# Optimization experiments

Hardware: AMD Instinct MI355X
Metric: run time of the kernel (lower is better)

Reference implementation:

```python
import jax, jax.numpy as jnp
import numpy as np
from functools import partial

BATCH, SEQ = 2, 2048
D_MODEL, D_INNER, D_XB = 2048, 4096, 1024
HEADDIM, D_STATE = 64, 64
NHEADS = D_INNER // HEADDIM      # 64
NKV = D_XB // HEADDIM            # 16
REP = NHEADS // NKV              # 4
INTER = 8192
EPS = 1e-5
D_IN_PROJ = D_INNER + D_XB + D_XB + D_INNER + NHEADS  # z, x, B, C, dt


def setup_inputs() -> dict:
    key = jax.random.key(0)
    ks = jax.random.split(key, 8)
    g = lambda k, shape, s: (jax.random.normal(k, shape, jnp.float32) * s)
    return {
        "hidden_states": g(ks[0], (BATCH, SEQ, D_MODEL), 1.0),
        "ln_w": jnp.ones((D_MODEL,), jnp.float32),
        "ln_b": jnp.zeros((D_MODEL,), jnp.float32),
        "in_proj_w": g(ks[1], (D_IN_PROJ, D_MODEL), 0.02),
        "dt_bias": jax.random.uniform(ks[2], (NHEADS,), jnp.float32, -4.0, 0.0),
        "A_log": jnp.log(jnp.arange(1, NHEADS + 1, dtype=jnp.float32)),
        "Dp": jnp.ones((NHEADS,), jnp.float32),
        "norm_w": jnp.ones((D_INNER,), jnp.float32),
        "out_proj_w": g(ks[3], (D_MODEL, D_INNER), 0.02),
        "fc1_w": g(ks[4], (INTER, D_MODEL), 0.02),
        "fc1_b": jnp.zeros((INTER,), jnp.float32),
        "fc2_w": g(ks[5], (D_MODEL, INTER), 0.02),
        "fc2_b": jnp.zeros((D_MODEL,), jnp.float32),
    }


def _layernorm(x, w, b):
    mu = x.mean(-1, keepdims=True)
    var = ((x - mu) ** 2).mean(-1, keepdims=True)
    return (x - mu) * jax.lax.rsqrt(var + EPS) * w + b


def _ssd_scan(xh, dt, A, Bh, Ch):
    # xh: (b,l,h,p)  dt: (b,l,h)  A: (h,)  Bh,Ch: (b,l,h,n)
    dA = jnp.exp(dt * A)  # (b,l,h) discrete decay
    to_l = lambda t: jnp.moveaxis(t, 1, 0)  # time-major for scan

    def step(state, inp):
        dA_t, dt_t, x_t, B_t, C_t = inp
        state = state * dA_t[:, :, None, None] + jnp.einsum(
            "bh,bhp,bhn->bhpn", dt_t, x_t, B_t)
        y = jnp.einsum("bhpn,bhn->bhp", state, C_t)
        return state, y

    state0 = jnp.zeros((xh.shape[0], NHEADS, HEADDIM, D_STATE), xh.dtype)
    _, ys = jax.lax.scan(step, state0, (to_l(dA), to_l(dt), to_l(xh), to_l(Bh), to_l(Ch)))
    return jnp.moveaxis(ys, 0, 1)  # (b,l,h,p)


def reference(hidden_states, ln_w, ln_b, in_proj_w, dt_bias, A_log, Dp,
              norm_w, out_proj_w, fc1_w, fc1_b, fc2_w, fc2_b):
    residual = hidden_states
    h = _layernorm(hidden_states, ln_w, ln_b)

    # ---- Mamba2 branch ----
    zxbcdt = h @ in_proj_w.T  # (b,l,D_IN_PROJ)
    z, x, Bm, Cm, dt = jnp.split(
        zxbcdt, np.cumsum([D_INNER, D_XB, D_XB, D_INNER]).tolist(), axis=-1)
    b, l = h.shape[0], h.shape[1]
    dt = jax.nn.softplus(dt + dt_bias)               # (b,l,nheads)
    A = -jnp.exp(A_log)                              # (nheads,)
    # GQA-style repeat of x (values) and B (keys) from NKV to NHEADS groups
    xh = jnp.repeat(x.reshape(b, l, NKV, HEADDIM), REP, axis=2)   # (b,l,h,p)
    Bh = jnp.repeat(Bm.reshape(b, l, NKV, D_STATE), REP, axis=2)  # (b,l,h,n)
    Ch = Cm.reshape(b, l, NHEADS, D_STATE)                        # (b,l,h,n)

    y = _ssd_scan(xh, dt, A, Bh, Ch) + Dp[None, None, :, None] * xh
    yf = y.reshape(b, l, D_INNER)
    # gated RMSNorm (norm_before_gate=False): gate first, then rmsnorm
    yf = yf * jax.nn.silu(z)
    yf = yf * jax.lax.rsqrt((yf * yf).mean(-1, keepdims=True) + EPS) * norm_w
    mamba_out = yf @ out_proj_w.T

    # ---- Phi MLP branch (parallel, shares the layernormed input) ----
    mlp = jax.nn.gelu(h @ fc1_w.T + fc1_b, approximate=True) @ fc2_w.T + fc2_b

    # resid_dropout is identity in eval mode
    return mamba_out + mlp + residual
```

## Files before the change

### kernel.cpp

```cpp
#include <hip/hip_runtime.h>
#include <hip/hip_bf16.h>

#define BATCH 2
#define SEQ   2048
#define DMODEL 2048
#define DINNER 4096
#define DXB   1024
#define NHEADS 64
#define NKV   16
#define HEADDIM 64
#define DSTATE 64
#define INTER 8192
#define DINPROJ 10304
#define ROWS  (BATCH*SEQ)
#define NC    32
#define EPSV  1e-5f

typedef short short8 __attribute__((ext_vector_type(8)));
typedef float f32x4 __attribute__((ext_vector_type(4)));

typedef const __attribute__((address_space(1))) unsigned int cg_u32;
typedef __attribute__((address_space(3))) unsigned int ls_u32;

static __device__ __forceinline__ void gll16(const void* g, void* l) {
    __builtin_amdgcn_global_load_lds((cg_u32*)g, (ls_u32*)l, 16, 0, 0);
}

static __device__ __forceinline__ unsigned short f2bf(float f) {
    unsigned int u = __float_as_uint(f);
    unsigned int r = (u + 0x7fffu + ((u >> 16) & 1u)) >> 16;
    return (unsigned short)r;
}
static __device__ __forceinline__ float bf2f(unsigned short h) {
    return __uint_as_float(((unsigned int)h) << 16);
}

__global__ __launch_bounds__(256) void convk(const float* __restrict__ in,
                                             unsigned short* __restrict__ out, int n4) {
    int stride = gridDim.x * blockDim.x;
    for (int i = blockIdx.x * blockDim.x + threadIdx.x; i < n4; i += stride) {
        float4 v = ((const float4*)in)[i];
        ushort4 o;
        o.x = f2bf(v.x); o.y = f2bf(v.y); o.z = f2bf(v.z); o.w = f2bf(v.w);
        ((ushort4*)out)[i] = o;
    }
}

__global__ __launch_bounds__(256) void ln_kernel(const float* __restrict__ x,
                                                 const float* __restrict__ w,
                                                 const float* __restrict__ b,
                                                 unsigned short* __restrict__ hout) {
    int row = blockIdx.x;
    int t = threadIdx.x;
    const float* xr = x + (size_t)row * DMODEL;
    float v[8];
    float4 v0 = *(const float4*)&xr[t * 8];
    float4 v1 = *(const float4*)&xr[t * 8 + 4];
    v[0]=v0.x; v[1]=v0.y; v[2]=v0.z; v[3]=v0.w; v[4]=v1.x; v[5]=v1.y; v[6]=v1.z; v[7]=v1.w;
    float s = 0.f, s2 = 0.f;
    #pragma unroll
    for (int i = 0; i < 8; ++i) { s += v[i]; s2 += v[i]*v[i]; }
    #pragma unroll
    for (int off = 1; off < 64; off <<= 1) { s += __shfl_xor(s, off); s2 += __shfl_xor(s2, off); }
    __shared__ float sa[4], sb[4];
    int lane = t & 63, wv = t >> 6;
    if (lane == 0) { sa[wv] = s; sb[wv] = s2; }
    __syncthreads();
    s = sa[0]+sa[1]+sa[2]+sa[3];
    s2 = sb[0]+sb[1]+sb[2]+sb[3];
    float mu = s / DMODEL;
    float var = s2 / DMODEL - mu * mu;
    float sc = rsqrtf(var + EPSV);
    unsigned short* ho = hout + (size_t)row * DMODEL + t * 8;
    #pragma unroll
    for (int i = 0; i < 8; ++i) {
        int d = t * 8 + i;
        ho[i] = f2bf((v[i] - mu) * sc * w[d] + b[d]);
    }
}

#define SLOTSZ 49152
template <int EPI>
__global__ __launch_bounds__(512, 2) void gemm_p(
    const unsigned short* __restrict__ A, const unsigned short* __restrict__ B,
    int M, int N, int K, int nby,
    float* __restrict__ outF, unsigned short* __restrict__ outH,
    const float* __restrict__ bias, const float* __restrict__ add1,
    const float* __restrict__ add2) {
    __shared__ __align__(16) char smem[3 * SLOTSZ];
    int t = threadIdx.x, lane = t & 63, w = t >> 6;
    int nwg = gridDim.x, cpx = nwg >> 3;
    int logical = (blockIdx.x & 7) * cpx + (blockIdx.x >> 3);
    int by = logical % nby, bx = logical / nby;
    int brow = by * 128, bcol = bx * 256;
    int wr = w >> 2, wc = w & 3;
    int wrb = wr * 64, wcb = wc * 64;

    int lr8 = lane >> 3;
    int lch = ((lane & 7) ^ lr8) << 3;
    const unsigned short* pa[2];
    #pragma unroll
    for (int j = 0; j < 2; ++j)
        pa[j] = A + (size_t)(brow + w * 16 + j * 8 + lr8) * K + lch;
    const unsigned short* pb[4];
    #pragma unroll
    for (int j = 0; j < 4; ++j) {
        int r = bcol + w * 32 + j * 8 + lr8;
        if (r > N - 1) r = N - 1;
        pb[j] = B + (size_t)r * K + lch;
    }
    auto stageA = [&](int slot, int j) {
        gll16(pa[j], smem + slot * SLOTSZ + (w * 16 + j * 8) * 128);
        pa[j] += 64;
    };
    auto stageB = [&](int slot, int j) {
        gll16(pb[j], smem + slot * SLOTSZ + 16384 + (w * 32 + j * 8) * 128);
        pb[j] += 64;
    };

    int arow = lane & 15;
    int swz0 = (((lane >> 4) ^ (lane & 7)) << 4);

    f32x4 acc[4][4] = {};
    const int NT = K >> 6;
    #pragma unroll
    for (int j = 0; j < 2; ++j) stageA(0, j);
    #pragma unroll
    for (int j = 0; j < 4; ++j) stageB(0, j);
    #pragma unroll
    for (int j = 0; j < 2; ++j) stageA(1, j);
    #pragma unroll
    for (int j = 0; j < 4; ++j) stageB(1, j);

    int slot = 0, slot2 = 2;
    for (int kt = 0; kt < NT; ++kt) {
        if (kt + 1 < NT) { asm volatile("s_waitcnt vmcnt(6)" ::: "memory"); }
        else             { asm volatile("s_waitcnt vmcnt(0)" ::: "memory"); }
        __builtin_amdgcn_s_barrier();
        asm volatile("" ::: "memory");
        const char* Ab = smem + slot * SLOTSZ;
        const char* Bb = Ab + 16384;
        bool st = (kt + 2 < NT);
        short8 af[4], bfv[4];
        #pragma unroll
        for (int f = 0; f < 4; ++f)
            af[f] = *(const short8*)(Ab + (wrb + f * 16 + arow) * 128 + swz0);
        #pragma unroll
        for (int n = 0; n < 4; ++n)
            bfv[n] = *(const short8*)(Bb + (wcb + n * 16 + arow) * 128 + swz0);
        if (st) { stageA(slot2, 0); stageA(slot2, 1); stageB(slot2, 0); }
        __builtin_amdgcn_s_setprio(1);
        #pragma unroll
        for (int f = 0; f < 4; ++f)
            #pragma unroll
            for (int n = 0; n < 4; ++n)
                acc[f][n] = __builtin_amdgcn_mfma_f32_16x16x32_bf16(af[f], bfv[n], acc[f][n], 0, 0, 0);
        __builtin_amdgcn_s_setprio(0);
        #pragma unroll
        for (int f = 0; f < 4; ++f)
            af[f] = *(const short8*)(Ab + (wrb + f * 16 + arow) * 128 + (swz0 ^ 64));
        #pragma unroll
        for (int n = 0; n < 4; ++n)
            bfv[n] = *(const short8*)(Bb + (wcb + n * 16 + arow) * 128 + (swz0 ^ 64));
        if (st) { stageB(slot2, 1); stageB(slot2, 2); stageB(slot2, 3); }
        __builtin_amdgcn_s_setprio(1);
        #pragma unroll
        for (int f = 0; f < 4; ++f)
            #pragma unroll
            for (int n = 0; n < 4; ++n)
                acc[f][n] = __builtin_amdgcn_mfma_f32_16x16x32_bf16(af[f], bfv[n], acc[f][n], 0, 0, 0);
        __builtin_amdgcn_s_setprio(0);
        slot  = (slot  == 2) ? 0 : slot + 1;
        slot2 = (slot2 == 2) ? 0 : slot2 + 1;
    }

    int rlane = (lane >> 4) << 2, clane = lane & 15;
    #pragma unroll
    for (int f = 0; f < 4; ++f) {
        #pragma unroll
        for (int n = 0; n < 4; ++n) {
            int col = bcol + wcb + n * 16 + clane;
            if (col < N) {
                #pragma unroll
                for (int j = 0; j < 4; ++j) {
                    int row = brow + wrb + f * 16 + rlane + j;
                    size_t idx = (size_t)row * N + col;
                    float v = acc[f][n][j];
                    if constexpr (EPI == 0) {
                        outF[idx] = v;
                    } else if constexpr (EPI == 1) {
                        v += bias[col];
                        float g = 0.5f * v * (1.f + tanhf(0.7978845608f * (v + 0.044715f * v * v * v)));
                        outH[idx] = f2bf(g);
                    } else if constexpr (EPI == 2) {
                        outF[idx] = v + bias[col] + add1[idx] + add2[idx];
                    } else {
                        outH[idx] = f2bf(v);
                    }
                }
            }
        }
    }
}

static __device__ __forceinline__ void mm64(const unsigned short* Al, const unsigned short* Bl,
                                            f32x4* acc, int w, int lane) {
    int lr = lane & 15, kg = (lane >> 4) << 3;
    #pragma unroll
    for (int ks = 0; ks < 2; ++ks) {
        short8 a = *(const short8*)&Al[(w * 16 + lr) * 64 + ks * 32 + kg];
        #pragma unroll
        for (int fn = 0; fn < 4; ++fn) {
            short8 bb = *(const short8*)&Bl[(fn * 16 + lr) * 64 + ks * 32 + kg];
            acc[fn] = __builtin_amdgcn_mfma_f32_16x16x32_bf16(a, bb, acc[fn], 0, 0, 0);
        }
    }
}

__global__ __launch_bounds__(256) void chunk_front(const unsigned short* __restrict__ zx,
                                                   const float* __restrict__ dt_bias,
                                                   const float* __restrict__ A_log,
                                                   float* __restrict__ pcum,
                                                   unsigned short* __restrict__ ybuf,
                                                   unsigned short* __restrict__ Sbuf) {
    __shared__ __align__(16) unsigned short Cs[64*64], Bsr[64*64], Btr[64*64],
                                            Xtr[64*64], Xw[64*64], Wsm[64*64];
    __shared__ float dts[64], clg[64];
    int t = threadIdx.x, lane = t & 63, w = t >> 6;
    int bid = blockIdx.x;
    int c = bid & 31, h = (bid >> 5) & 63, b = bid >> 11, g = h >> 2;
    int row0 = (b << 11) + (c << 6);

    if (t < 64) {
        float raw = bf2f(zx[(size_t)(row0 + t) * DINPROJ + 10240 + h]) + dt_bias[h];
        float dt = raw > 20.f ? raw : log1pf(expf(raw));
        dts[t] = dt;
        float v = dt * (-expf(A_log[h]));
        #pragma unroll
        for (int off = 1; off < 64; off <<= 1) {
            float o = __shfl_up(v, off);
            if (lane >= off) v += o;
        }
        clg[t] = v;
        pcum[(size_t)(row0 + t) * 64 + h] = expf(v);
    }
    ushort4 xr[4];
    #pragma unroll
    for (int i = 0; i < 4; ++i) {
        int q = i * 256 + t, s = q >> 4, d4 = (q & 15) << 2;
        const unsigned short* rp = zx + (size_t)(row0 + s) * DINPROJ;
        ushort4 cv = *(const ushort4*)&rp[6144 + h * 64 + d4];
        *(ushort4*)&Cs[s * 64 + d4] = cv;
        ushort4 bv = *(const ushort4*)&rp[5120 + g * 64 + d4];
        *(ushort4*)&Bsr[s * 64 + d4] = bv;
        Btr[(d4 + 0) * 64 + s] = bv.x; Btr[(d4 + 1) * 64 + s] = bv.y;
        Btr[(d4 + 2) * 64 + s] = bv.z; Btr[(d4 + 3) * 64 + s] = bv.w;
        ushort4 xv = *(const ushort4*)&rp[4096 + g * 64 + d4];
        Xtr[(d4 + 0) * 64 + s] = xv.x; Xtr[(d4 + 1) * 64 + s] = xv.y;
        Xtr[(d4 + 2) * 64 + s] = xv.z; Xtr[(d4 + 3) * 64 + s] = xv.w;
        xr[i] = xv;
    }
    __syncthreads();
    float cl63 = clg[63];
    #pragma unroll
    for (int i = 0; i < 4; ++i) {
        int q = i * 256 + t, s = q >> 4, d4 = (q & 15) << 2;
        float ws = dts[s] * expf(cl63 - clg[s]);
        Xw[(d4 + 0) * 64 + s] = f2bf(bf2f(xr[i].x) * ws);
        Xw[(d4 + 1) * 64 + s] = f2bf(bf2f(xr[i].y) * ws);
        Xw[(d4 + 2) * 64 + s] = f2bf(bf2f(xr[i].z) * ws);
        Xw[(d4 + 3) * 64 + s] = f2bf(bf2f(xr[i].w) * ws);
    }
    __syncthreads();
    f32x4 accG[4] = {};
    mm64(Cs, Bsr, accG, w, lane);
    int rl = (lane >> 4) << 2, cl = lane & 15;
    #pragma unroll
    for (int fn = 0; fn < 4; ++fn) {
        #pragma unroll
        for (int j = 0; j < 4; ++j) {
            int tr = w * 16 + rl + j, rc = fn * 16 + cl;
            float val = 0.f;
            if (rc <= tr) val = accG[fn][j] * expf(clg[tr] - clg[rc]) * dts[rc];
            Wsm[tr * 64 + rc] = f2bf(val);
        }
    }
    __syncthreads();
    f32x4 accY[4] = {};
    mm64(Wsm, Xtr, accY, w, lane);
    f32x4 accS[4] = {};
    mm64(Xw, Btr, accS, w, lane);
    size_t cb = (size_t)((((b << 6) + h) << 5) + c) * 4096;
    #pragma unroll
    for (int fn = 0; fn < 4; ++fn) {
        #pragma unroll
        for (int j = 0; j < 4; ++j) {
            int tr = w * 16 + rl + j, pc = fn * 16 + cl;
            ybuf[(size_t)(row0 + tr) * DINNER + h * 64 + pc] = f2bf(accY[fn][j]);
            Sbuf[cb + tr * 64 + pc] = f2bf(accS[fn][j]);
        }
    }
}

__global__ __launch_bounds__(256) void chunk_state(unsigned short* __restrict__ SH,
                                                   const float* __restrict__ pcum) {
    int b = blockIdx.x >> 6, h = blockIdx.x & 63, t = threadIdx.x;
    float H[16];
    #pragma unroll
    for (int j = 0; j < 16; ++j) H[j] = 0.f;
    for (int c = 0; c < NC; ++c) {
        size_t base = (size_t)((((b << 6) + h) << 5) + c) * 4096;
        float Tc = pcum[(size_t)((b << 11) + (c << 6) + 63) * 64 + h];
        #pragma unroll
        for (int j = 0; j < 16; ++j) {
            int e = j * 256 + t;
            unsigned short sv = SH[base + e];
            SH[base + e] = f2bf(H[j]);
            H[j] = H[j] * Tc + bf2f(sv);
        }
    }
}

__global__ __launch_bounds__(256) void chunk_back(const unsigned short* __restrict__ zx,
                                                  const unsigned short* __restrict__ SH,
                                                  const float* __restrict__ pcum,
                                                  const float* __restrict__ Dp,
                                                  unsigned short* __restrict__ ybuf) {
    __shared__ __align__(16) unsigned short Cs[64*64], Hs[64*64];
    __shared__ float ps[64];
    int t = threadIdx.x, lane = t & 63, w = t >> 6;
    int bid = blockIdx.x;
    int c = bid & 31, h = (bid >> 5) & 63, b = bid >> 11, g = h >> 2;
    int row0 = (b << 11) + (c << 6);
    size_t cb = (size_t)((((b << 6) + h) << 5) + c) * 4096;
    #pragma unroll
    for (int i = 0; i < 4; ++i) {
        int q = i * 256 + t, s = q >> 4, d4 = (q & 15) << 2;
        *(ushort4*)&Cs[s * 64 + d4] =
            *(const ushort4*)&zx[(size_t)(row0 + s) * DINPROJ + 6144 + h * 64 + d4];
        *(ushort4*)&Hs[s * 64 + d4] = *(const ushort4*)&SH[cb + s * 64 + d4];
    }
    if (t < 64) ps[t] = pcum[(size_t)(row0 + t) * 64 + h];
    __syncthreads();
    f32x4 acc[4] = {};
    mm64(Cs, Hs, acc, w, lane);
    float Dph = Dp[h];
    int rl = (lane >> 4) << 2, cl = lane & 15;
    #pragma unroll
    for (int fn = 0; fn < 4; ++fn) {
        #pragma unroll
        for (int j = 0; j < 4; ++j) {
            int tr = w * 16 + rl + j, pc = fn * 16 + cl;
            size_t yi = (size_t)(row0 + tr) * DINNER + h * 64 + pc;
            float xv = bf2f(zx[(size_t)(row0 + tr) * DINPROJ + 4096 + g * 64 + pc]);
            ybuf[yi] = f2bf(bf2f(ybuf[yi]) + acc[fn][j] * ps[tr] + Dph * xv);
        }
    }
}

__global__ __launch_bounds__(256) void gate_kernel(const unsigned short* __restrict__ y,
                                                   const unsigned short* __restrict__ zx,
                                                   const float* __restrict__ norm_w,
                                                   unsigned short* __restrict__ yf) {
    int row = blockIdx.x;
    int t = threadIdx.x;
    float v[16];
    float s2 = 0.f;
    #pragma unroll
    for (int i = 0; i < 16; ++i) {
        int d = i * 256 + t;
        float yv = bf2f(y[(size_t)row * DINNER + d]);
        float zv = bf2f(zx[(size_t)row * DINPROJ + d]);
        float gt = zv / (1.f + expf(-zv));
        v[i] = yv * gt;
        s2 += v[i] * v[i];
    }
    #pragma unroll
    for (int off = 1; off < 64; off <<= 1) s2 += __shfl_xor(s2, off);
    __shared__ float sb[4];
    int lane = t & 63, wv = t >> 6;
    if (lane == 0) sb[wv] = s2;
    __syncthreads();
    s2 = sb[0] + sb[1] + sb[2] + sb[3];
    float sc = rsqrtf(s2 / DINNER + EPSV);
    #pragma unroll
    for (int i = 0; i < 16; ++i) {
        int d = i * 256 + t;
        yf[(size_t)row * DINNER + d] = f2bf(v[i] * sc * norm_w[d]);
    }
}

extern "C" void kernel_launch(void* const* d_in, const int* in_sizes, int n_in,
                              void* d_out, int out_size, void* d_ws, size_t ws_size,
                              hipStream_t stream) {
    const float* hid   = (const float*)d_in[0];
    const float* ln_w  = (const float*)d_in[1];
    const float* ln_b  = (const float*)d_in[2];
    const float* w_inp = (const float*)d_in[3];
    const float* dtb   = (const float*)d_in[4];
    const float* A_log = (const float*)d_in[5];
    const float* Dp    = (const float*)d_in[6];
    const float* nw    = (const float*)d_in[7];
    const float* w_out = (const float*)d_in[8];
    const float* w_fc1 = (const float*)d_in[9];
    const float* fc1_b = (const float*)d_in[10];
    const float* w_fc2 = (const float*)d_in[11];
    const float* fc2_b = (const float*)d_in[12];

    char* ws = (char*)d_ws;
    size_t off = 0;
    auto alloc = [&](size_t bytes) { size_t o = off; off += (bytes + 255) & ~(size_t)255; return o; };
    size_t o_h    = alloc((size_t)ROWS * DMODEL * 2);
    size_t o_w    = alloc((size_t)DINPROJ * DMODEL * 2);
    size_t o_zx   = alloc((size_t)ROWS * DINPROJ * 2);
    size_t o_pc   = alloc((size_t)ROWS * NHEADS * 4);
    size_t o_y    = alloc((size_t)ROWS * DINNER * 2);
    size_t o_yf   = alloc((size_t)ROWS * DINNER * 2);
    size_t o_S    = alloc((size_t)BATCH * NHEADS * NC * HEADDIM * DSTATE * 2);

    unsigned short* h_bf  = (unsigned short*)(ws + o_h);
    unsigned short* wbuf  = (unsigned short*)(ws + o_w);
    unsigned short* zx    = (unsigned short*)(ws + o_zx);
    float* pcum           = (float*)(ws + o_pc);
    unsigned short* ybuf  = (unsigned short*)(ws + o_y);
    unsigned short* yf    = (unsigned short*)(ws + o_yf);
    unsigned short* Sbuf  = (unsigned short*)(ws + o_S);
    unsigned short* gelu  = (unsigned short*)(ws + o_zx);
    float* mamba          = (float*)(ws + o_y);
    float* outF           = (float*)d_out;

    ln_kernel<<<ROWS, 256, 0, stream>>>(hid, ln_w, ln_b, h_bf);
    convk<<<2048, 256, 0, stream>>>(w_inp, wbuf, (DINPROJ * DMODEL) / 4);
    gemm_p<3><<<41 * 32, 512, 0, stream>>>(
        h_bf, wbuf, ROWS, DINPROJ, DMODEL, 32, nullptr, zx, nullptr, nullptr, nullptr);
    chunk_front<<<BATCH * NHEADS * NC, 256, 0, stream>>>(zx, dtb, A_log, pcum, ybuf, Sbuf);
    chunk_state<<<BATCH * NHEADS, 256, 0, stream>>>(Sbuf, pcum);
    chunk_back<<<BATCH * NHEADS * NC, 256, 0, stream>>>(zx, Sbuf, pcum, Dp, ybuf);
    gate_kernel<<<ROWS, 256, 0, stream>>>(ybuf, zx, nw, yf);
    convk<<<2048, 256, 0, stream>>>(w_out, wbuf, (DMODEL * DINNER) / 4);
    gemm_p<0><<<8 * 32, 512, 0, stream>>>(
        yf, wbuf, ROWS, DMODEL, DINNER, 32, mamba, nullptr, nullptr, nullptr, nullptr);
    convk<<<2048, 256, 0, stream>>>(w_fc1, wbuf, (INTER * DMODEL) / 4);
    gemm_p<1><<<32 * 32, 512, 0, stream>>>(
        h_bf, wbuf, ROWS, INTER, DMODEL, 32, nullptr, gelu, fc1_b, nullptr, nullptr);
    convk<<<2048, 256, 0, stream>>>(w_fc2, wbuf, (DMODEL * INTER) / 4);
    gemm_p<2><<<8 * 32, 512, 0, stream>>>(
        gelu, wbuf, ROWS, DMODEL, INTER, 32, outF, nullptr, fc2_b, mamba, hid);
}
```

Baseline: 792.1 us.

## Fold weight fp32-to-bf16 conversions into tails of preceding kernels

Removes the four standalone weight-conversion launches. Each conversion now runs as a grid-stride loop at the end of an earlier kernel (layernorm, in-proj GEMM, chunk_front, out-proj GEMM), writing into its own dedicated bf16 weight buffer. The aim is to save launch overhead and let the memory-bound conversion overlap with the tail or under-occupied phases of compute kernels. In exchange it uses more workspace, and the extra code and work may add register pressure or lengthen the GEMM kernels.

```diff
diff --git a/kernel.cpp b/kernel.cpp
--- a/kernel.cpp
+++ b/kernel.cpp
@@ -35,21 +35,24 @@
     return __uint_as_float(((unsigned int)h) << 16);
 }
 
-__global__ __launch_bounds__(256) void convk(const float* __restrict__ in,
-                                             unsigned short* __restrict__ out, int n4) {
-    int stride = gridDim.x * blockDim.x;
-    for (int i = blockIdx.x * blockDim.x + threadIdx.x; i < n4; i += stride) {
-        float4 v = ((const float4*)in)[i];
+static __device__ __forceinline__ void conv_gs(const float* __restrict__ src,
+                                               unsigned short* __restrict__ dst,
+                                               int n4, int gtid, int gstride) {
+    if (!src) return;
+    for (int i = gtid; i < n4; i += gstride) {
+        float4 v = ((const float4*)src)[i];
         ushort4 o;
         o.x = f2bf(v.x); o.y = f2bf(v.y); o.z = f2bf(v.z); o.w = f2bf(v.w);
-        ((ushort4*)out)[i] = o;
+        ((ushort4*)dst)[i] = o;
     }
 }
 
 __global__ __launch_bounds__(256) void ln_kernel(const float* __restrict__ x,
                                                  const float* __restrict__ w,
                                                  const float* __restrict__ b,
-                                                 unsigned short* __restrict__ hout) {
+                                                 unsigned short* __restrict__ hout,
+                                                 const float* __restrict__ csrc,
+                                                 unsigned short* __restrict__ cdst, int cn4) {
     int row = blockIdx.x;
     int t = threadIdx.x;
     const float* xr = x + (size_t)row * DMODEL;
@@ -77,6 +80,7 @@
         int d = t * 8 + i;
         ho[i] = f2bf((v[i] - mu) * sc * w[d] + b[d]);
     }
+    conv_gs(csrc, cdst, cn4, blockIdx.x * 256 + t, gridDim.x * 256);
 }
 
 #define SLOTSZ 49152
@@ -86,7 +90,8 @@
     int M, int N, int K, int nby,
     float* __restrict__ outF, unsigned short* __restrict__ outH,
     const float* __restrict__ bias, const float* __restrict__ add1,
-    const float* __restrict__ add2) {
+    const float* __restrict__ add2,
+    const float* __restrict__ csrc, unsigned short* __restrict__ cdst, int cn4) {
     __shared__ __align__(16) char smem[3 * SLOTSZ];
     int t = threadIdx.x, lane = t & 63, w = t >> 6;
     int nwg = gridDim.x, cpx = nwg >> 3;
@@ -201,6 +206,7 @@
             }
         }
     }
+    conv_gs(csrc, cdst, cn4, (int)blockIdx.x * 512 + t, nwg * 512);
 }
 
 static __device__ __forceinline__ void mm64(const unsigned short* Al, const unsigned short* Bl,
@@ -222,7 +228,9 @@
                                                    const float* __restrict__ A_log,
                                                    float* __restrict__ pcum,
                                                    unsigned short* __restrict__ ybuf,
-                                                   unsigned short* __restrict__ Sbuf) {
+                                                   unsigned short* __restrict__ Sbuf,
+                                                   const float* __restrict__ csrc,
+                                                   unsigned short* __restrict__ cdst, int cn4) {
     __shared__ __align__(16) unsigned short Cs[64*64], Bsr[64*64], Btr[64*64],
                                             Xtr[64*64], Xw[64*64], Wsm[64*64];
     __shared__ float dts[64], clg[64];
@@ -300,6 +308,7 @@
             Sbuf[cb + tr * 64 + pc] = f2bf(accS[fn][j]);
         }
     }
+    conv_gs(csrc, cdst, cn4, bid * 256 + t, (int)gridDim.x * 256);
 }
 
 __global__ __launch_bounds__(256) void chunk_state(unsigned short* __restrict__ SH,
@@ -411,7 +420,10 @@
     size_t off = 0;
     auto alloc = [&](size_t bytes) { size_t o = off; off += (bytes + 255) & ~(size_t)255; return o; };
     size_t o_h    = alloc((size_t)ROWS * DMODEL * 2);
-    size_t o_w    = alloc((size_t)DINPROJ * DMODEL * 2);
+    size_t o_wi   = alloc((size_t)DINPROJ * DMODEL * 2);
+    size_t o_wo   = alloc((size_t)DMODEL * DINNER * 2);
+    size_t o_wf1  = alloc((size_t)INTER * DMODEL * 2);
+    size_t o_wf2  = alloc((size_t)DMODEL * INTER * 2);
     size_t o_zx   = alloc((size_t)ROWS * DINPROJ * 2);
     size_t o_pc   = alloc((size_t)ROWS * NHEADS * 4);
     size_t o_y    = alloc((size_t)ROWS * DINNER * 2);
@@ -419,7 +431,10 @@
     size_t o_S    = alloc((size_t)BATCH * NHEADS * NC * HEADDIM * DSTATE * 2);
 
     unsigned short* h_bf  = (unsigned short*)(ws + o_h);
-    unsigned short* wbuf  = (unsigned short*)(ws + o_w);
+    unsigned short* wbi   = (unsigned short*)(ws + o_wi);
+    unsigned short* wbo   = (unsigned short*)(ws + o_wo);
+    unsigned short* wbf1  = (unsigned short*)(ws + o_wf1);
+    unsigned short* wbf2  = (unsigned short*)(ws + o_wf2);
     unsigned short* zx    = (unsigned short*)(ws + o_zx);
     float* pcum           = (float*)(ws + o_pc);
     unsigned short* ybuf  = (unsigned short*)(ws + o_y);
@@ -429,21 +444,23 @@
     float* mamba          = (float*)(ws + o_y);
     float* outF           = (float*)d_out;
 
-    ln_kernel<<<ROWS, 256, 0, stream>>>(hid, ln_w, ln_b, h_bf);
-    convk<<<2048, 256, 0, stream>>>(w_inp, wbuf, (DINPROJ * DMODEL) / 4);
+    ln_kernel<<<ROWS, 256, 0, stream>>>(hid, ln_w, ln_b, h_bf,
+                                        w_inp, wbi, (DINPROJ * DMODEL) / 4);
     gemm_p<3><<<41 * 32, 512, 0, stream>>>(
-        h_bf, wbuf, ROWS, DINPROJ, DMODEL, 32, nullptr, zx, nullptr, nullptr, nullptr);
-    chunk_front<<<BATCH * NHEADS * NC, 256, 0, stream>>>(zx, dtb, A_log, pcum, ybuf, Sbuf);
+        h_bf, wbi, ROWS, DINPROJ, DMODEL, 32, nullptr, zx, nullptr, nullptr, nullptr,
+        w_out, wbo, (DMODEL * DINNER) / 4);
+    chunk_front<<<BATCH * NHEADS * NC, 256, 0, stream>>>(zx, dtb, A_log, pcum, ybuf, Sbuf,
+                                                         w_fc1, wbf1, (INTER * DMODEL) / 4);
     chunk_state<<<BATCH * NHEADS, 256, 0, stream>>>(Sbuf, pcum);
     chunk_back<<<BATCH * NHEADS * NC, 256, 0, stream>>>(zx, Sbuf, pcum, Dp, ybuf);
     gate_kernel<<<ROWS, 256, 0, stream>>>(ybuf, zx, nw, yf);
-    convk<<<2048, 256, 0, stream>>>(w_out, wbuf, (DMODEL * DINNER) / 4);
     gemm_p<0><<<8 * 32, 512, 0, stream>>>(
-        yf, wbuf, ROWS, DMODEL, DINNER, 32, mamba, nullptr, nullptr, nullptr, nullptr);
-    convk<<<2048, 256, 0, stream>>>(w_fc1, wbuf, (INTER * DMODEL) / 4);
+        yf, wbo, ROWS, DMODEL, DINNER, 32, mamba, nullptr, nullptr, nullptr, nullptr,
+        w_fc2, wbf2, (DMODEL * INTER) / 4);
     gemm_p<1><<<32 * 32, 512, 0, stream>>>(
-        h_bf, wbuf, ROWS, INTER, DMODEL, 32, nullptr, gelu, fc1_b, nullptr, nullptr);
-    convk<<<2048, 256, 0, stream>>>(w_fc2, wbuf, (DMODEL * INTER) / 4);
+        h_bf, wbf1, ROWS, INTER, DMODEL, 32, nullptr, gelu, fc1_b, nullptr, nullptr,
+        nullptr, nullptr, 0);
     gemm_p<2><<<8 * 32, 512, 0, stream>>>(
-        gelu, wbuf, ROWS, DMODEL, INTER, 32, outF, nullptr, fc2_b, mamba, hid);
-}
+        gelu, wbf2, ROWS, DMODEL, INTER, 32, outF, nullptr, fc2_b, mamba, hid,
+        nullptr, nullptr, 0);
+}
```

Measured after the change: 823.2 us. +3.9%, slower.
